# Optimization experiments

Hardware: AMD Instinct MI355X
Metric: run time of the kernel (lower is better)

The kernel has to match this reference:

```python
import jax, jax.numpy as jnp
import numpy as np

NEG = -9e15
SLOPE = 0.1  # LeakyReLU negative_slope in the torch module

B, N, NFEAT = 4, 2048, 256
NHID, NHEADS, NOUT = 64, 8, 128


def setup_inputs() -> dict:
    key = jax.random.key(0)
    ks = jax.random.split(key, 8)
    x = jax.random.normal(ks[0], (B, N, NFEAT), dtype=jnp.float32)
    adj = jax.random.randint(ks[1], (B, N, N), 0, 2, dtype=jnp.int32)
    s = 0.1
    Wh = jax.random.normal(ks[2], (NHEADS, NFEAT, NHID), dtype=jnp.float32) * s
    ah = jax.random.normal(ks[3], (NHEADS, 2 * NHID), dtype=jnp.float32) * s
    bh = jax.random.normal(ks[4], (NHEADS, NHID), dtype=jnp.float32) * s
    Wo = jax.random.normal(ks[5], (NHID * NHEADS, NOUT), dtype=jnp.float32) * s
    ao = jax.random.normal(ks[6], (2 * NOUT,), dtype=jnp.float32) * s
    bo = jax.random.normal(ks[7], (NOUT,), dtype=jnp.float32) * s
    return {"x": x, "adj": adj, "Wh": Wh, "ah": ah, "bh": bh,
            "Wo": Wo, "ao": ao, "bo": bo}


def _leaky(v):
    return jnp.where(v >= 0, v, SLOPE * v)


def _gat_layer(x, adj, W, a, b):
    # x: [B,N,Fin], W: [Fin,F], a: [2F], b: [F]
    h = jnp.einsum('bnf,fo->bno', x, W)          # [B,N,F]
    F = W.shape[1]
    a1, a2 = a[:F], a[F:]
    s1 = h @ a1                                   # [B,N] (query / row term)
    s2 = h @ a2                                   # [B,N] (key / col term)
    e = _leaky(s1[:, :, None] + s2[:, None, :])   # [B,N,N], avoids a_input blowup
    e = jnp.where(adj > 0, e, NEG)
    att = jax.nn.softmax(e, axis=2)               # [B,N,N]
    h_prime = jnp.einsum('bnm,bmf->bnf', att, h) + b
    return jax.nn.elu(h_prime)


def reference(x, adj, Wh, ah, bh, Wo, ao, bo):
    # per-head layers, vmapped over the head axis of the stacked params
    heads = jax.vmap(lambda W, a, b: _gat_layer(x, adj, W, a, b))(Wh, ah, bh)
    # [H,B,N,F] -> concat heads along feature dim: [B,N,H*F]
    hcat = jnp.transpose(heads, (1, 2, 0, 3)).reshape(x.shape[0], x.shape[1], -1)
    out = _gat_layer(hcat, adj, Wo, ao, bo)
    return jax.nn.relu(out)
```

## Files before the change

kernel.cpp:

```cpp
#include <hip/hip_runtime.h>

constexpr int B_ = 4;
constexpr int N_ = 2048;
constexpr int NFEAT_ = 256;
constexpr int NHEADS_ = 8;
constexpr float SLOPE_ = 0.1f;
constexpr float L2E = 1.4426950408889634f;

typedef __attribute__((ext_vector_type(8))) __fp16 f16x8;
typedef __attribute__((ext_vector_type(4))) __fp16 f16x4;
typedef __attribute__((ext_vector_type(2))) __fp16 f16x2;
typedef __attribute__((ext_vector_type(4))) float f32x4;

__device__ __forceinline__ f16x8 pack8(const float* v) {
  union { f16x2 h2[4]; f16x8 h8; } u;
  u.h2[0] = __builtin_amdgcn_cvt_pkrtz(v[0], v[1]);
  u.h2[1] = __builtin_amdgcn_cvt_pkrtz(v[2], v[3]);
  u.h2[2] = __builtin_amdgcn_cvt_pkrtz(v[4], v[5]);
  u.h2[3] = __builtin_amdgcn_cvt_pkrtz(v[6], v[7]);
  return u.h8;
}
__device__ __forceinline__ f16x4 pack4(float a, float b, float c, float d) {
  union { f16x2 h2[2]; f16x4 h4; } u;
  u.h2[0] = __builtin_amdgcn_cvt_pkrtz(a, b);
  u.h2[1] = __builtin_amdgcn_cvt_pkrtz(c, d);
  return u.h4;
}

__global__ __launch_bounds__(256) void k_prep(
    const int* __restrict__ adj, unsigned short* __restrict__ mask2,
    const float* __restrict__ Wh, __fp16* __restrict__ WhB,
    const float* __restrict__ Wo, __fp16* __restrict__ WoB)
{
  const int bid = blockIdx.x;
  const int l = threadIdx.x & 63;
  if (bid < 4096) {
    const size_t gw = ((size_t)bid * 256 + threadIdx.x) >> 6;
    const int jt = (int)(gw & 31);
    const int ig16 = (int)((gw >> 5) & 127);
    const int b = (int)(gw >> 12);
    const int q = l >> 4, c15 = l & 15;
    const int* base = adj + ((size_t)b * N_ + ig16 * 16) * N_ + jt * 64 + l;
    unsigned int msk = 0;
    #pragma unroll
    for (int r = 0; r < 16; ++r) {
      int a = base[(size_t)r * N_];
      unsigned long long bal = __ballot(a > 0);
      unsigned int v = (unsigned int)((bal >> (q * 8)) & 0xffull)
                     | ((unsigned int)((bal >> (q * 8 + 32)) & 0xffull) << 8);
      if (r == c15) msk = v;
    }
    mask2[gw * 64 + l] = (unsigned short)msk;
  } else if (bid < 4160) {
    int s = (int)(((bid - 4096) * 256 + threadIdx.x) >> 6);
    int h = s >> 5, ks = (s >> 2) & 7, ft = s & 3;
    const float* src = Wh + ((size_t)h * 256 + ks * 32 + (l >> 4) * 8) * 64 + ft * 16 + (l & 15);
    float v[8];
    #pragma unroll
    for (int j = 0; j < 8; ++j) v[j] = src[(size_t)j * 64];
    *(f16x8*)(WhB + (size_t)s * 512 + l * 8) = pack8(v);
  } else {
    int s = (int)(((bid - 4160) * 256 + threadIdx.x) >> 6);
    int ks = s >> 3, ft = s & 7;
    const float* src = Wo + ((size_t)ks * 32 + (l >> 4) * 8) * 128 + ft * 16 + (l & 15);
    float v[8];
    #pragma unroll
    for (int j = 0; j < 8; ++j) v[j] = src[(size_t)j * 128];
    *(f16x8*)(WoB + (size_t)s * 512 + l * 8) = pack8(v);
  }
}

__global__ __launch_bounds__(256, 4) void k_gemm1(
    const float* __restrict__ x, const __fp16* __restrict__ WhB,
    const float* __restrict__ ah,
    __fp16* __restrict__ hB1, float* __restrict__ s1h, float* __restrict__ s2h)
{
  constexpr int XP = 264;
  __shared__ __fp16 xs[16 * XP];
  __shared__ __fp16 hT[512 * 16];

  const int t = threadIdx.x;
  const int bid = blockIdx.x;
  const int b = bid >> 7;
  const int n0 = (bid & 127) * 16;

  {
    int r = t >> 4, k0 = (t & 15) * 16;
    const float* src = x + ((size_t)(b * N_) + n0 + r) * NFEAT_ + k0;
    float v0[8], v1[8];
    *(float4*)&v0[0] = *(const float4*)(src);
    *(float4*)&v0[4] = *(const float4*)(src + 4);
    *(float4*)&v1[0] = *(const float4*)(src + 8);
    *(float4*)&v1[4] = *(const float4*)(src + 12);
    *(f16x8*)&xs[r * XP + k0] = pack8(v0);
    *(f16x8*)&xs[r * XP + k0 + 8] = pack8(v1);
  }
  __syncthreads();

  const int w = t >> 6, l = t & 63;
  const int quad = l >> 4, c15 = l & 15;

  f32x4 acc[8];
  #pragma unroll
  for (int i = 0; i < 8; ++i) acc[i] = (f32x4){0.f, 0.f, 0.f, 0.f};

  for (int ks = 0; ks < 8; ++ks) {
    f16x8 af = *(const f16x8*)&xs[c15 * XP + ks * 32 + quad * 8];
    #pragma unroll
    for (int tt = 0; tt < 8; ++tt) {
      int hl = tt >> 2, ft = tt & 3;
      f16x8 bf = *(const f16x8*)(WhB +
          ((((size_t)(2 * w + hl) * 8 + ks) * 4 + ft) * 512) + l * 8);
      acc[tt] = __builtin_amdgcn_mfma_f32_16x16x32_f16(af, bf, acc[tt], 0, 0, 0);
    }
  }

  #pragma unroll
  for (int hl = 0; hl < 2; ++hl) {
    int head = 2 * w + hl;
    float a1v[4], a2v[4];
    #pragma unroll
    for (int ft = 0; ft < 4; ++ft) {
      a1v[ft] = ah[head * 128 + ft * 16 + c15] * L2E;
      a2v[ft] = ah[head * 128 + 64 + ft * 16 + c15] * L2E;
    }
    #pragma unroll
    for (int r = 0; r < 4; ++r) {
      float v1 = 0.f, v2 = 0.f;
      #pragma unroll
      for (int ft = 0; ft < 4; ++ft) {
        v1 = fmaf(acc[hl * 4 + ft][r], a1v[ft], v1);
        v2 = fmaf(acc[hl * 4 + ft][r], a2v[ft], v2);
      }
      #pragma unroll
      for (int off = 1; off < 16; off <<= 1) {
        v1 += __shfl_xor(v1, off, 64);
        v2 += __shfl_xor(v2, off, 64);
      }
      if (c15 == 0) {
        s1h[(size_t)(b * NHEADS_ + head) * N_ + n0 + quad * 4 + r] = v1;
        s2h[(size_t)(b * NHEADS_ + head) * N_ + n0 + quad * 4 + r] = v2;
      }
    }
  }

  #pragma unroll
  for (int tt = 0; tt < 8; ++tt) {
    int f = (2 * w + (tt >> 2)) * 64 + (tt & 3) * 16 + c15;
    *(f16x4*)&hT[f * 16 + quad * 4] =
        pack4(acc[tt][0], acc[tt][1], acc[tt][2], acc[tt][3]);
  }
  __syncthreads();

  const int base_oct = (n0 >> 3) & 3;
  #pragma unroll
  for (int q = 0; q < 4; ++q) {
    int s = t + q * 256;
    int c15v = s & 15, oct = (s >> 4) & 1, ft = (s >> 5) & 3, head = s >> 7;
    f16x8 v = *(const f16x8*)&hT[(head * 64 + ft * 16 + c15v) * 16 + oct * 8];
    int lane0 = (base_oct + oct) * 16 + c15v;
    *(f16x8*)(hB1 +
        ((((size_t)(b * NHEADS_ + head) * 64 + (n0 >> 5)) * 4 + ft) * 512) + lane0 * 8) = v;
  }
}

__global__ __launch_bounds__(256, 4) void k_gemm2(
    const __fp16* __restrict__ g1, const __fp16* __restrict__ WoB,
    const float* __restrict__ ao,
    __fp16* __restrict__ hB2, float* __restrict__ s1o, float* __restrict__ s2o)
{
  constexpr int GP = 520;
  __shared__ __fp16 gs[16 * GP];
  __shared__ __fp16 hT[128 * 16];
  __shared__ float sd1[4][16], sd2[4][16];

  const int t = threadIdx.x;
  const int bid = blockIdx.x;
  const int b = bid >> 7;
  const int n0 = (bid & 127) * 16;

  {
    int r = t >> 4, k0 = (t & 15) * 32;
    const __fp16* src = g1 + ((size_t)(b * N_) + n0 + r) * 512 + k0;
    #pragma unroll
    for (int i = 0; i < 4; ++i)
      *(f16x8*)&gs[r * GP + k0 + i * 8] = *(const f16x8*)(src + i * 8);
  }
  __syncthreads();

  const int w = t >> 6, l = t & 63;
  const int quad = l >> 4, c15 = l & 15;

  f32x4 acc[2];
  acc[0] = (f32x4){0.f, 0.f, 0.f, 0.f};
  acc[1] = (f32x4){0.f, 0.f, 0.f, 0.f};

  for (int ks = 0; ks < 16; ++ks) {
    f16x8 af = *(const f16x8*)&gs[c15 * GP + ks * 32 + quad * 8];
    #pragma unroll
    for (int tt = 0; tt < 2; ++tt) {
      int ft = 2 * w + tt;
      f16x8 bf = *(const f16x8*)(WoB + (((size_t)ks * 8 + ft) * 512) + l * 8);
      acc[tt] = __builtin_amdgcn_mfma_f32_16x16x32_f16(af, bf, acc[tt], 0, 0, 0);
    }
  }

  {
    float a1v[2], a2v[2];
    #pragma unroll
    for (int tt = 0; tt < 2; ++tt) {
      int f = (2 * w + tt) * 16 + c15;
      a1v[tt] = ao[f] * L2E;
      a2v[tt] = ao[128 + f] * L2E;
    }
    #pragma unroll
    for (int r = 0; r < 4; ++r) {
      float v1 = acc[0][r] * a1v[0] + acc[1][r] * a1v[1];
      float v2 = acc[0][r] * a2v[0] + acc[1][r] * a2v[1];
      #pragma unroll
      for (int off = 1; off < 16; off <<= 1) {
        v1 += __shfl_xor(v1, off, 64);
        v2 += __shfl_xor(v2, off, 64);
      }
      if (c15 == 0) { sd1[w][quad * 4 + r] = v1; sd2[w][quad * 4 + r] = v2; }
    }
  }

  #pragma unroll
  for (int tt = 0; tt < 2; ++tt) {
    int f = (2 * w + tt) * 16 + c15;
    *(f16x4*)&hT[f * 16 + quad * 4] =
        pack4(acc[tt][0], acc[tt][1], acc[tt][2], acc[tt][3]);
  }
  __syncthreads();

  if (t < 16)
    s1o[(size_t)b * N_ + n0 + t] = sd1[0][t] + sd1[1][t] + sd1[2][t] + sd1[3][t];
  else if (t < 32) {
    int rr = t - 16;
    s2o[(size_t)b * N_ + n0 + rr] = sd2[0][rr] + sd2[1][rr] + sd2[2][rr] + sd2[3][rr];
  }

  {
    int c15v = t & 15, oct = (t >> 4) & 1, ft = t >> 5;
    f16x8 v = *(const f16x8*)&hT[(ft * 16 + c15v) * 16 + oct * 8];
    int base_oct = (n0 >> 3) & 3;
    int lane0 = (base_oct + oct) * 16 + c15v;
    *(f16x8*)(hB2 +
        (((size_t)(b * 64 + (n0 >> 5)) * 8 + ft) * 512) + lane0 * 8) = v;
  }
}

__global__ __launch_bounds__(512, 4) void k_att1(
    const __fp16* __restrict__ hB, const float* __restrict__ s1,
    const float* __restrict__ s2, const unsigned short* __restrict__ mask2,
    const float* __restrict__ bias, __fp16* __restrict__ g1)
{
  constexpr int NRG = 4, NJQ = 2, JLEN = 1024, TJ = 64, NIT = JLEN / TJ;
  constexpr int TILE = TJ * 64;

  __shared__ __fp16 vbuf[NJQ][2][TILE];
  __shared__ float s2s[N_];
  __shared__ float red[8];

  const int tid = threadIdx.x;
  const int w = tid >> 6, l = tid & 63;
  const int quad = l >> 4, c15 = l & 15;
  const int rowg = w % NRG, jq = w / NRG;
  const int tc = rowg * 64 + l;

  int idx = blockIdx.x;
  const int ig = idx & 31; idx >>= 5;
  const int head = idx & 7;
  const int b = idx >> 3;
  const int i0w = ig * 64 + rowg * 16;

  const float* s1p = s1 + (size_t)(b * 8 + head) * N_;
  const float* s2p = s2 + (size_t)(b * 8 + head) * N_;
  const char* hBp = (const char*)(hB + (size_t)(b * 8 + head) * (N_ / 32) * 2048);
  const unsigned short* mp = mask2 + ((size_t)(b * 128 + (i0w >> 4)) * 32) * 64 + l;

  const int jbase = jq * JLEN;

  auto stage = [&](int j0, int slot) {
    const char* srcb = hBp + (size_t)(j0 >> 5) * 4096;
    #pragma unroll
    for (int c = 0; c < 2; ++c) {
      int off = (tc + c * 256) * 16;
      __builtin_amdgcn_global_load_lds(
          (const __attribute__((address_space(1))) unsigned int*)(srcb + off),
          (__attribute__((address_space(3))) unsigned int*)
              ((char*)&vbuf[jq][slot][0] + (off - l * 16)), 16, 0, 0);
    }
  };

  stage(jbase, 0);
  unsigned int mk = mp[(size_t)(jbase >> 6) * 64];

  float4 sv = *(const float4*)(s2p + tid * 4);
  *(float4*)&s2s[tid * 4] = sv;
  float lm = fmaxf(fmaxf(sv.x, sv.y), fmaxf(sv.z, sv.w));
  #pragma unroll
  for (int off = 1; off < 64; off <<= 1) lm = fmaxf(lm, __shfl_xor(lm, off, 64));
  if (l == 0) red[w] = lm;
  const float s1v = s1p[i0w + c15];
  __syncthreads();
  float s2m = red[0];
  #pragma unroll
  for (int q = 1; q < 8; ++q) s2m = fmaxf(s2m, red[q]);

  const float zm = s1v + s2m;
  const float m = fmaxf(zm, SLOPE_ * zm);
  const float p = s1v - m;
  const float cq = (SLOPE_ - 1.f) * m;

  f16x8 ones;
  #pragma unroll
  for (int i = 0; i < 8; ++i) ones[i] = (__fp16)1.0f;

  f32x4 acc[4], acc5;
  #pragma unroll
  for (int t = 0; t < 4; ++t) acc[t] = (f32x4){0.f, 0.f, 0.f, 0.f};
  acc5 = (f32x4){0.f, 0.f, 0.f, 0.f};

  for (int it = 0; it < NIT; ++it) {
    const int cur = it & 1;
    const int j0 = jbase + it * TJ;
    unsigned int nk = 0;
    if (it + 1 < NIT) {
      stage(j0 + TJ, cur ^ 1);
      nk = mp[(size_t)((j0 + TJ) >> 6) * 64];
    }

    #pragma unroll
    for (int h = 0; h < 2; ++h) {
      const int jk = j0 + h * 32;
      float s2r[8];
      *(float4*)&s2r[0] = *(const float4*)&s2s[jk + quad * 8];
      *(float4*)&s2r[4] = *(const float4*)&s2s[jk + quad * 8 + 4];
      const unsigned int mbyte = (mk >> (8 * h)) & 0xffu;
      float wgt[8];
      #pragma unroll
      for (int k = 0; k < 8; ++k) {
        float t0 = p + s2r[k];
        float t1 = fmaf(SLOPE_, t0, cq);
        float tm = fmaxf(t0, t1);
        float e = __builtin_amdgcn_exp2f(tm);
        int sel = (int)(mbyte << (31 - k)) >> 31;
        union { float f; int i; } u; u.f = e; u.i &= sel;
        wgt[k] = u.f;
      }
      f16x8 a = pack8(wgt);
      acc5 = __builtin_amdgcn_mfma_f32_16x16x32_f16(a, ones, acc5, 0, 0, 0);
      const __fp16* vb = &vbuf[jq][cur][h * 2048];
      #pragma unroll
      for (int t = 0; t < 4; ++t) {
        f16x8 bf = *(const f16x8*)(vb + t * 512 + l * 8);
        acc[t] = __builtin_amdgcn_mfma_f32_16x16x32_f16(a, bf, acc[t], 0, 0, 0);
      }
    }
    mk = nk;
    __syncthreads();
  }

  auto pacc = (float(*)[16][64])(&vbuf[0][0][0]);
  auto pls  = (float(*)[16])(&s2s[0]);
  if (jq == 1) {
    #pragma unroll
    for (int t = 0; t < 4; ++t)
      #pragma unroll
      for (int r = 0; r < 4; ++r)
        pacc[rowg][quad * 4 + r][t * 16 + c15] = acc[t][r];
    if (c15 == 0) {
      #pragma unroll
      for (int r = 0; r < 4; ++r) pls[rowg][quad * 4 + r] = acc5[r];
    }
  }
  __syncthreads();
  if (jq == 0) {
    float Lrow[4];
    #pragma unroll
    for (int r = 0; r < 4; ++r)
      Lrow[r] = acc5[r] + pls[rowg][quad * 4 + r];
    #pragma unroll
    for (int t = 0; t < 4; ++t)
      #pragma unroll
      for (int r = 0; r < 4; ++r)
        acc[t][r] += pacc[rowg][quad * 4 + r][t * 16 + c15];
    float lr[4];
    #pragma unroll
    for (int r = 0; r < 4; ++r) lr[r] = 1.f / Lrow[r];
    #pragma unroll
    for (int t = 0; t < 4; ++t) {
      const float bv = bias[head * 64 + t * 16 + c15];
      #pragma unroll
      for (int r = 0; r < 4; ++r) {
        const int i = i0w + quad * 4 + r;
        float v = acc[t][r] * lr[r] + bv;
        v = (v > 0.f) ? v : expm1f(v);
        g1[(size_t)(b * N_ + i) * 512 + head * 64 + t * 16 + c15] = (__fp16)v;
      }
    }
  }
}

__global__ __launch_bounds__(512, 4) void k_att2(
    const __fp16* __restrict__ hB, const float* __restrict__ s1,
    const float* __restrict__ s2, const unsigned short* __restrict__ mask2,
    const float* __restrict__ bias, float* __restrict__ out)
{
  constexpr int NRG = 2, NJQ = 4, JLEN = 512, TJ = 32, NIT = JLEN / TJ;

  __shared__ float s2s[N_];
  __shared__ float red[8];
  __shared__ float paccS[NJQ - 1][NRG][16][64];
  __shared__ float pls[NJQ - 1][NRG][16];

  const int tid = threadIdx.x;
  const int w = tid >> 6, l = tid & 63;
  const int quad = l >> 4, c15 = l & 15;
  const int rowg = w % NRG, jq = w / NRG;

  int idx = blockIdx.x;
  const int ig = idx & 63; idx >>= 6;
  const int fs = idx & 1;
  const int b = idx >> 1;
  const int i0w = ig * 32 + rowg * 16;

  const float* s1p = s1 + (size_t)b * N_;
  const float* s2p = s2 + (size_t)b * N_;
  const __fp16* hBp = hB + (size_t)b * 64 * 4096 + fs * 2048 + (size_t)l * 8;
  const unsigned short* mp = mask2 + ((size_t)(b * 128 + (i0w >> 4)) * 32) * 64 + l;

  float4 sv = *(const float4*)(s2p + tid * 4);
  *(float4*)&s2s[tid * 4] = sv;
  float lm = fmaxf(fmaxf(sv.x, sv.y), fmaxf(sv.z, sv.w));
  #pragma unroll
  for (int off = 1; off < 64; off <<= 1) lm = fmaxf(lm, __shfl_xor(lm, off, 64));
  if (l == 0) red[w] = lm;
  const float s1v = s1p[i0w + c15];
  __syncthreads();
  float s2m = red[0];
  #pragma unroll
  for (int q = 1; q < 8; ++q) s2m = fmaxf(s2m, red[q]);

  const float zm = s1v + s2m;
  const float m = fmaxf(zm, SLOPE_ * zm);
  const float p = s1v - m;
  const float cq = (SLOPE_ - 1.f) * m;

  f16x8 ones;
  #pragma unroll
  for (int i = 0; i < 8; ++i) ones[i] = (__fp16)1.0f;

  f32x4 acc[4], acc5;
  #pragma unroll
  for (int t = 0; t < 4; ++t) acc[t] = (f32x4){0.f, 0.f, 0.f, 0.f};
  acc5 = (f32x4){0.f, 0.f, 0.f, 0.f};

  const int jbase = jq * JLEN;
  unsigned int mk = mp[(size_t)(jbase >> 6) * 64];

  for (int it = 0; it < NIT; ++it) {
    const int j0 = jbase + it * TJ;
    const __fp16* vb = hBp + (size_t)(j0 >> 5) * 4096;
    f16x8 bf0 = *(const f16x8*)(vb);
    f16x8 bf1 = *(const f16x8*)(vb + 512);
    f16x8 bf2 = *(const f16x8*)(vb + 1024);
    f16x8 bf3 = *(const f16x8*)(vb + 1536);

    float s2r[8];
    *(float4*)&s2r[0] = *(const float4*)&s2s[j0 + quad * 8];
    *(float4*)&s2r[4] = *(const float4*)&s2s[j0 + quad * 8 + 4];
    const unsigned int mbyte = (mk >> (8 * (it & 1))) & 0xffu;
    if (it & 1) mk = mp[(size_t)((j0 + TJ) >> 6) * 64];

    float wgt[8];
    #pragma unroll
    for (int k = 0; k < 8; ++k) {
      float t0 = p + s2r[k];
      float t1 = fmaf(SLOPE_, t0, cq);
      float tm = fmaxf(t0, t1);
      float e = __builtin_amdgcn_exp2f(tm);
      int sel = (int)(mbyte << (31 - k)) >> 31;
      union { float f; int i; } u; u.f = e; u.i &= sel;
      wgt[k] = u.f;
    }
    f16x8 a = pack8(wgt);
    acc5 = __builtin_amdgcn_mfma_f32_16x16x32_f16(a, ones, acc5, 0, 0, 0);
    acc[0] = __builtin_amdgcn_mfma_f32_16x16x32_f16(a, bf0, acc[0], 0, 0, 0);
    acc[1] = __builtin_amdgcn_mfma_f32_16x16x32_f16(a, bf1, acc[1], 0, 0, 0);
    acc[2] = __builtin_amdgcn_mfma_f32_16x16x32_f16(a, bf2, acc[2], 0, 0, 0);
    acc[3] = __builtin_amdgcn_mfma_f32_16x16x32_f16(a, bf3, acc[3], 0, 0, 0);
  }

  if (jq > 0) {
    #pragma unroll
    for (int t = 0; t < 4; ++t)
      #pragma unroll
      for (int r = 0; r < 4; ++r)
        paccS[jq - 1][rowg][quad * 4 + r][t * 16 + c15] = acc[t][r];
    if (c15 == 0) {
      #pragma unroll
      for (int r = 0; r < 4; ++r) pls[jq - 1][rowg][quad * 4 + r] = acc5[r];
    }
  }
  __syncthreads();
  if (jq == 0) {
    float Lrow[4];
    #pragma unroll
    for (int r = 0; r < 4; ++r) Lrow[r] = acc5[r];
    #pragma unroll
    for (int q = 0; q < NJQ - 1; ++q) {
      #pragma unroll
      for (int t = 0; t < 4; ++t)
        #pragma unroll
        for (int r = 0; r < 4; ++r)
          acc[t][r] += paccS[q][rowg][quad * 4 + r][t * 16 + c15];
      #pragma unroll
      for (int r = 0; r < 4; ++r) Lrow[r] += pls[q][rowg][quad * 4 + r];
    }
    float lr[4];
    #pragma unroll
    for (int r = 0; r < 4; ++r) lr[r] = 1.f / Lrow[r];
    #pragma unroll
    for (int t = 0; t < 4; ++t) {
      const float bv = bias[fs * 64 + t * 16 + c15];
      #pragma unroll
      for (int r = 0; r < 4; ++r) {
        const int i = i0w + quad * 4 + r;
        float v = acc[t][r] * lr[r] + bv;
        out[(size_t)(b * N_ + i) * 128 + fs * 64 + t * 16 + c15] = fmaxf(v, 0.f);
      }
    }
  }
}

extern "C" void kernel_launch(void* const* d_in, const int* in_sizes, int n_in,
                              void* d_out, int out_size, void* d_ws, size_t ws_size,
                              hipStream_t stream) {
  const float* x   = (const float*)d_in[0];
  const int*   adj = (const int*)d_in[1];
  const float* Wh  = (const float*)d_in[2];
  const float* ah  = (const float*)d_in[3];
  const float* bh  = (const float*)d_in[4];
  const float* Wo  = (const float*)d_in[5];
  const float* ao  = (const float*)d_in[6];
  const float* bo  = (const float*)d_in[7];
  float* out = (float*)d_out;

  float* ws   = (float*)d_ws;
  float* s1h  = ws;
  float* s2h  = s1h  + (size_t)B_ * NHEADS_ * N_;
  float* s1o  = s2h  + (size_t)B_ * NHEADS_ * N_;
  float* s2o  = s1o  + (size_t)B_ * N_;
  __fp16* g1  = (__fp16*)(s2o + (size_t)B_ * N_);
  __fp16* hB1 = g1  + (size_t)B_ * N_ * 512;
  __fp16* hB2 = hB1 + (size_t)B_ * NHEADS_ * N_ * 64;
  __fp16* WhB = hB2 + (size_t)B_ * N_ * 128;
  __fp16* WoB = WhB + (size_t)8 * 256 * 64;
  unsigned short* mask2 = (unsigned short*)(WoB + (size_t)512 * 128);

  k_prep<<<4192, 256, 0, stream>>>(adj, mask2, Wh, WhB, Wo, WoB);
  k_gemm1<<<B_ * (N_ / 16), 256, 0, stream>>>(x, WhB, ah, hB1, s1h, s2h);
  k_att1<<<B_ * NHEADS_ * (N_ / 64), 512, 0, stream>>>(
      hB1, s1h, s2h, mask2, bh, g1);
  k_gemm2<<<B_ * (N_ / 16), 256, 0, stream>>>(g1, WoB, ao, hB2, s1o, s2o);
  k_att2<<<B_ * 2 * (N_ / 32), 512, 0, stream>>>(
      hB2, s1o, s2o, mask2, bo, out);
}
```

Baseline: 197.7 us.

## Split projection GEMMs across more blocks by head pair and feature half

The first projection kernel now launches one block per (batch, row tile, head pair) instead of per (batch, row tile). Each wave computes two 16-column tiles of one head rather than eight, which quadruples the grid and cuts per-wave accumulator registers. The second projection kernel is split in two along output features, and the partial s1/s2 attention scores are written to two separate buffers that the final attention kernel sums. The aim is more parallelism for these small GEMMs. The cost is that each x tile is loaded and converted redundantly per head pair, and g1 rows are reread twice.

```diff
diff --git a/kernel.cpp b/kernel.cpp
--- a/kernel.cpp
+++ b/kernel.cpp
@@ -77,12 +77,15 @@
 {
   constexpr int XP = 264;
   __shared__ __fp16 xs[16 * XP];
-  __shared__ __fp16 hT[512 * 16];
+  __shared__ __fp16 hT[128 * 16];
+  __shared__ float sd1[4][16], sd2[4][16];
 
   const int t = threadIdx.x;
   const int bid = blockIdx.x;
-  const int b = bid >> 7;
-  const int n0 = (bid & 127) * 16;
+  const int hp = bid & 3;
+  const int ng = (bid >> 2) & 127;
+  const int b  = bid >> 9;
+  const int n0 = ng * 16;
 
   {
     int r = t >> 4, k0 = (t & 15) * 16;
@@ -99,108 +102,20 @@
 
   const int w = t >> 6, l = t & 63;
   const int quad = l >> 4, c15 = l & 15;
-
-  f32x4 acc[8];
-  #pragma unroll
-  for (int i = 0; i < 8; ++i) acc[i] = (f32x4){0.f, 0.f, 0.f, 0.f};
-
-  for (int ks = 0; ks < 8; ++ks) {
-    f16x8 af = *(const f16x8*)&xs[c15 * XP + ks * 32 + quad * 8];
-    #pragma unroll
-    for (int tt = 0; tt < 8; ++tt) {
-      int hl = tt >> 2, ft = tt & 3;
-      f16x8 bf = *(const f16x8*)(WhB +
-          ((((size_t)(2 * w + hl) * 8 + ks) * 4 + ft) * 512) + l * 8);
-      acc[tt] = __builtin_amdgcn_mfma_f32_16x16x32_f16(af, bf, acc[tt], 0, 0, 0);
-    }
-  }
-
-  #pragma unroll
-  for (int hl = 0; hl < 2; ++hl) {
-    int head = 2 * w + hl;
-    float a1v[4], a2v[4];
-    #pragma unroll
-    for (int ft = 0; ft < 4; ++ft) {
-      a1v[ft] = ah[head * 128 + ft * 16 + c15] * L2E;
-      a2v[ft] = ah[head * 128 + 64 + ft * 16 + c15] * L2E;
-    }
-    #pragma unroll
-    for (int r = 0; r < 4; ++r) {
-      float v1 = 0.f, v2 = 0.f;
-      #pragma unroll
-      for (int ft = 0; ft < 4; ++ft) {
-        v1 = fmaf(acc[hl * 4 + ft][r], a1v[ft], v1);
-        v2 = fmaf(acc[hl * 4 + ft][r], a2v[ft], v2);
-      }
-      #pragma unroll
-      for (int off = 1; off < 16; off <<= 1) {
-        v1 += __shfl_xor(v1, off, 64);
-        v2 += __shfl_xor(v2, off, 64);
-      }
-      if (c15 == 0) {
-        s1h[(size_t)(b * NHEADS_ + head) * N_ + n0 + quad * 4 + r] = v1;
-        s2h[(size_t)(b * NHEADS_ + head) * N_ + n0 + quad * 4 + r] = v2;
-      }
-    }
-  }
-
-  #pragma unroll
-  for (int tt = 0; tt < 8; ++tt) {
-    int f = (2 * w + (tt >> 2)) * 64 + (tt & 3) * 16 + c15;
-    *(f16x4*)&hT[f * 16 + quad * 4] =
-        pack4(acc[tt][0], acc[tt][1], acc[tt][2], acc[tt][3]);
-  }
-  __syncthreads();
-
-  const int base_oct = (n0 >> 3) & 3;
-  #pragma unroll
-  for (int q = 0; q < 4; ++q) {
-    int s = t + q * 256;
-    int c15v = s & 15, oct = (s >> 4) & 1, ft = (s >> 5) & 3, head = s >> 7;
-    f16x8 v = *(const f16x8*)&hT[(head * 64 + ft * 16 + c15v) * 16 + oct * 8];
-    int lane0 = (base_oct + oct) * 16 + c15v;
-    *(f16x8*)(hB1 +
-        ((((size_t)(b * NHEADS_ + head) * 64 + (n0 >> 5)) * 4 + ft) * 512) + lane0 * 8) = v;
-  }
-}
-
-__global__ __launch_bounds__(256, 4) void k_gemm2(
-    const __fp16* __restrict__ g1, const __fp16* __restrict__ WoB,
-    const float* __restrict__ ao,
-    __fp16* __restrict__ hB2, float* __restrict__ s1o, float* __restrict__ s2o)
-{
-  constexpr int GP = 520;
-  __shared__ __fp16 gs[16 * GP];
-  __shared__ __fp16 hT[128 * 16];
-  __shared__ float sd1[4][16], sd2[4][16];
-
-  const int t = threadIdx.x;
-  const int bid = blockIdx.x;
-  const int b = bid >> 7;
-  const int n0 = (bid & 127) * 16;
-
-  {
-    int r = t >> 4, k0 = (t & 15) * 32;
-    const __fp16* src = g1 + ((size_t)(b * N_) + n0 + r) * 512 + k0;
-    #pragma unroll
-    for (int i = 0; i < 4; ++i)
-      *(f16x8*)&gs[r * GP + k0 + i * 8] = *(const f16x8*)(src + i * 8);
-  }
-  __syncthreads();
-
-  const int w = t >> 6, l = t & 63;
-  const int quad = l >> 4, c15 = l & 15;
+  const int hl = w >> 1, fp = w & 1;
+  const int head = hp * 2 + hl;
 
   f32x4 acc[2];
   acc[0] = (f32x4){0.f, 0.f, 0.f, 0.f};
   acc[1] = (f32x4){0.f, 0.f, 0.f, 0.f};
 
-  for (int ks = 0; ks < 16; ++ks) {
-    f16x8 af = *(const f16x8*)&gs[c15 * GP + ks * 32 + quad * 8];
+  for (int ks = 0; ks < 8; ++ks) {
+    f16x8 af = *(const f16x8*)&xs[c15 * XP + ks * 32 + quad * 8];
     #pragma unroll
     for (int tt = 0; tt < 2; ++tt) {
-      int ft = 2 * w + tt;
-      f16x8 bf = *(const f16x8*)(WoB + (((size_t)ks * 8 + ft) * 512) + l * 8);
+      int ft = fp * 2 + tt;
+      f16x8 bf = *(const f16x8*)(WhB +
+          ((((size_t)head * 8 + ks) * 4 + ft) * 512) + l * 8);
       acc[tt] = __builtin_amdgcn_mfma_f32_16x16x32_f16(af, bf, acc[tt], 0, 0, 0);
     }
   }
@@ -209,9 +124,9 @@
     float a1v[2], a2v[2];
     #pragma unroll
     for (int tt = 0; tt < 2; ++tt) {
-      int f = (2 * w + tt) * 16 + c15;
-      a1v[tt] = ao[f] * L2E;
-      a2v[tt] = ao[128 + f] * L2E;
+      int ft = fp * 2 + tt;
+      a1v[tt] = ah[head * 128 + ft * 16 + c15] * L2E;
+      a2v[tt] = ah[head * 128 + 64 + ft * 16 + c15] * L2E;
     }
     #pragma unroll
     for (int r = 0; r < 4; ++r) {
@@ -228,26 +143,106 @@
 
   #pragma unroll
   for (int tt = 0; tt < 2; ++tt) {
-    int f = (2 * w + tt) * 16 + c15;
-    *(f16x4*)&hT[f * 16 + quad * 4] =
+    int fl = hl * 64 + (fp * 2 + tt) * 16 + c15;
+    *(f16x4*)&hT[fl * 16 + quad * 4] =
         pack4(acc[tt][0], acc[tt][1], acc[tt][2], acc[tt][3]);
   }
   __syncthreads();
 
   if (t < 16)
-    s1o[(size_t)b * N_ + n0 + t] = sd1[0][t] + sd1[1][t] + sd1[2][t] + sd1[3][t];
+    s1h[(size_t)(b * 8 + hp * 2) * N_ + n0 + t] = sd1[0][t] + sd1[1][t];
+  else if (t < 32) { int r = t - 16;
+    s2h[(size_t)(b * 8 + hp * 2) * N_ + n0 + r] = sd2[0][r] + sd2[1][r]; }
+  else if (t < 48) { int r = t - 32;
+    s1h[(size_t)(b * 8 + hp * 2 + 1) * N_ + n0 + r] = sd1[2][r] + sd1[3][r]; }
+  else if (t < 64) { int r = t - 48;
+    s2h[(size_t)(b * 8 + hp * 2 + 1) * N_ + n0 + r] = sd2[2][r] + sd2[3][r]; }
+
+  {
+    int c15v = t & 15, oct = (t >> 4) & 1, ftl = t >> 5;
+    int hl2 = ftl >> 2, ft = ftl & 3;
+    int headg = hp * 2 + hl2;
+    f16x8 v = *(const f16x8*)&hT[(ftl * 16 + c15v) * 16 + oct * 8];
+    int base_oct = (n0 >> 3) & 3;
+    int lane0 = (base_oct + oct) * 16 + c15v;
+    *(f16x8*)(hB1 +
+        ((((size_t)(b * 8 + headg) * 64 + (n0 >> 5)) * 4 + ft) * 512) + lane0 * 8) = v;
+  }
+}
+
+__global__ __launch_bounds__(256, 4) void k_gemm2(
+    const __fp16* __restrict__ g1, const __fp16* __restrict__ WoB,
+    const float* __restrict__ ao,
+    __fp16* __restrict__ hB2, float* __restrict__ s1oP, float* __restrict__ s2oP)
+{
+  constexpr int GP = 520;
+  __shared__ __fp16 gs[16 * GP];
+  __shared__ __fp16 hT[64 * 16];
+  __shared__ float sd1[4][16], sd2[4][16];
+
+  const int t = threadIdx.x;
+  const int bid = blockIdx.x;
+  const int fs = bid & 1;
+  const int ng = (bid >> 1) & 127;
+  const int b = bid >> 8;
+  const int n0 = ng * 16;
+
+  {
+    int r = t >> 4, k0 = (t & 15) * 32;
+    const __fp16* src = g1 + ((size_t)(b * N_) + n0 + r) * 512 + k0;
+    #pragma unroll
+    for (int i = 0; i < 4; ++i)
+      *(f16x8*)&gs[r * GP + k0 + i * 8] = *(const f16x8*)(src + i * 8);
+  }
+  __syncthreads();
+
+  const int w = t >> 6, l = t & 63;
+  const int quad = l >> 4, c15 = l & 15;
+  const int ft = fs * 4 + w;
+
+  f32x4 acc = (f32x4){0.f, 0.f, 0.f, 0.f};
+  for (int ks = 0; ks < 16; ++ks) {
+    f16x8 af = *(const f16x8*)&gs[c15 * GP + ks * 32 + quad * 8];
+    f16x8 bf = *(const f16x8*)(WoB + (((size_t)ks * 8 + ft) * 512) + l * 8);
+    acc = __builtin_amdgcn_mfma_f32_16x16x32_f16(af, bf, acc, 0, 0, 0);
+  }
+
+  {
+    float a1v = ao[ft * 16 + c15] * L2E;
+    float a2v = ao[128 + ft * 16 + c15] * L2E;
+    #pragma unroll
+    for (int r = 0; r < 4; ++r) {
+      float v1 = acc[r] * a1v, v2 = acc[r] * a2v;
+      #pragma unroll
+      for (int off = 1; off < 16; off <<= 1) {
+        v1 += __shfl_xor(v1, off, 64);
+        v2 += __shfl_xor(v2, off, 64);
+      }
+      if (c15 == 0) { sd1[w][quad * 4 + r] = v1; sd2[w][quad * 4 + r] = v2; }
+    }
+  }
+
+  *(f16x4*)&hT[(w * 16 + c15) * 16 + quad * 4] =
+      pack4(acc[0], acc[1], acc[2], acc[3]);
+  __syncthreads();
+
+  if (t < 16)
+    s1oP[(size_t)fs * (B_ * N_) + (size_t)b * N_ + n0 + t] =
+        sd1[0][t] + sd1[1][t] + sd1[2][t] + sd1[3][t];
   else if (t < 32) {
-    int rr = t - 16;
-    s2o[(size_t)b * N_ + n0 + rr] = sd2[0][rr] + sd2[1][rr] + sd2[2][rr] + sd2[3][rr];
-  }
-
-  {
-    int c15v = t & 15, oct = (t >> 4) & 1, ft = t >> 5;
-    f16x8 v = *(const f16x8*)&hT[(ft * 16 + c15v) * 16 + oct * 8];
+    int r = t - 16;
+    s2oP[(size_t)fs * (B_ * N_) + (size_t)b * N_ + n0 + r] =
+        sd2[0][r] + sd2[1][r] + sd2[2][r] + sd2[3][r];
+  }
+
+  if (t < 128) {
+    int c15v = t & 15, oct = (t >> 4) & 1, ftl = t >> 5;
+    int ftg = fs * 4 + ftl;
+    f16x8 v = *(const f16x8*)&hT[(ftl * 16 + c15v) * 16 + oct * 8];
     int base_oct = (n0 >> 3) & 3;
     int lane0 = (base_oct + oct) * 16 + c15v;
     *(f16x8*)(hB2 +
-        (((size_t)(b * 64 + (n0 >> 5)) * 8 + ft) * 512) + lane0 * 8) = v;
+        (((size_t)(b * 64 + (n0 >> 5)) * 8 + ftg) * 512) + lane0 * 8) = v;
   }
 }
 
@@ -405,8 +400,8 @@
 }
 
 __global__ __launch_bounds__(512, 4) void k_att2(
-    const __fp16* __restrict__ hB, const float* __restrict__ s1,
-    const float* __restrict__ s2, const unsigned short* __restrict__ mask2,
+    const __fp16* __restrict__ hB, const float* __restrict__ s1P,
+    const float* __restrict__ s2P, const unsigned short* __restrict__ mask2,
     const float* __restrict__ bias, float* __restrict__ out)
 {
   constexpr int NRG = 2, NJQ = 4, JLEN = 512, TJ = 32, NIT = JLEN / TJ;
@@ -427,18 +422,23 @@
   const int b = idx >> 1;
   const int i0w = ig * 32 + rowg * 16;
 
-  const float* s1p = s1 + (size_t)b * N_;
-  const float* s2p = s2 + (size_t)b * N_;
+  const float* s1p0 = s1P + (size_t)b * N_;
+  const float* s1p1 = s1P + (size_t)B_ * N_ + (size_t)b * N_;
+  const float* s2p0 = s2P + (size_t)b * N_;
+  const float* s2p1 = s2P + (size_t)B_ * N_ + (size_t)b * N_;
   const __fp16* hBp = hB + (size_t)b * 64 * 4096 + fs * 2048 + (size_t)l * 8;
   const unsigned short* mp = mask2 + ((size_t)(b * 128 + (i0w >> 4)) * 32) * 64 + l;
 
-  float4 sv = *(const float4*)(s2p + tid * 4);
+  float4 svA = *(const float4*)(s2p0 + tid * 4);
+  float4 svB = *(const float4*)(s2p1 + tid * 4);
+  float4 sv = make_float4(svA.x + svB.x, svA.y + svB.y,
+                          svA.z + svB.z, svA.w + svB.w);
   *(float4*)&s2s[tid * 4] = sv;
   float lm = fmaxf(fmaxf(sv.x, sv.y), fmaxf(sv.z, sv.w));
   #pragma unroll
   for (int off = 1; off < 64; off <<= 1) lm = fmaxf(lm, __shfl_xor(lm, off, 64));
   if (l == 0) red[w] = lm;
-  const float s1v = s1p[i0w + c15];
+  const float s1v = s1p0[i0w + c15] + s1p1[i0w + c15];
   __syncthreads();
   float s2m = red[0];
   #pragma unroll
@@ -552,9 +552,9 @@
   float* ws   = (float*)d_ws;
   float* s1h  = ws;
   float* s2h  = s1h  + (size_t)B_ * NHEADS_ * N_;
-  float* s1o  = s2h  + (size_t)B_ * NHEADS_ * N_;
-  float* s2o  = s1o  + (size_t)B_ * N_;
-  __fp16* g1  = (__fp16*)(s2o + (size_t)B_ * N_);
+  float* s1oP = s2h  + (size_t)B_ * NHEADS_ * N_;
+  float* s2oP = s1oP + (size_t)2 * B_ * N_;
+  __fp16* g1  = (__fp16*)(s2oP + (size_t)2 * B_ * N_);
   __fp16* hB1 = g1  + (size_t)B_ * N_ * 512;
   __fp16* hB2 = hB1 + (size_t)B_ * NHEADS_ * N_ * 64;
   __fp16* WhB = hB2 + (size_t)B_ * N_ * 128;
@@ -562,10 +562,10 @@
   unsigned short* mask2 = (unsigned short*)(WoB + (size_t)512 * 128);
 
   k_prep<<<4192, 256, 0, stream>>>(adj, mask2, Wh, WhB, Wo, WoB);
-  k_gemm1<<<B_ * (N_ / 16), 256, 0, stream>>>(x, WhB, ah, hB1, s1h, s2h);
+  k_gemm1<<<B_ * 128 * 4, 256, 0, stream>>>(x, WhB, ah, hB1, s1h, s2h);
   k_att1<<<B_ * NHEADS_ * (N_ / 64), 512, 0, stream>>>(
       hB1, s1h, s2h, mask2, bh, g1);
-  k_gemm2<<<B_ * (N_ / 16), 256, 0, stream>>>(g1, WoB, ao, hB2, s1o, s2o);
+  k_gemm2<<<B_ * 128 * 2, 256, 0, stream>>>(g1, WoB, ao, hB2, s1oP, s2oP);
   k_att2<<<B_ * 2 * (N_ / 32), 512, 0, stream>>>(
-      hB2, s1o, s2o, mask2, bo, out);
-}
+      hB2, s1oP, s2oP, mask2, bo, out);
+}
```

Result: no change. 199.4 us (+0.9%).
